# Kernel optimization log

Measured on AMD Instinct MI355X. Metric: run time of the kernel, lower is better.

## Reference

```python
import jax, jax.numpy as jnp
import numpy as np

ALPHA = 0.5        # damping from conf['alpha']
MAX_ITERS = 30     # fixed-point iterations (conf uses up to 150 with eps early-exit)
GN_GROUPS = 3
GN_EPS = 1e-5
SLOPE = 0.01       # F.leaky_relu default negative_slope


def _conv(x, w, b, pad):
    y = jax.lax.conv_general_dilated(
        x, w, window_strides=(1, 1), padding=[(pad, pad), (pad, pad)],
        dimension_numbers=("NCHW", "OIHW", "NCHW"))
    return y + b[None, :, None, None]


def _leaky(x):
    return jnp.where(x >= 0, x, SLOPE * x)


def _groupnorm(x, gamma, beta):
    N, C, H, W = x.shape
    xg = x.reshape(N, GN_GROUPS, C // GN_GROUPS, H, W)
    mu = xg.mean(axis=(2, 3, 4), keepdims=True)
    var = xg.var(axis=(2, 3, 4), keepdims=True)
    xg = (xg - mu) * jax.lax.rsqrt(var + GN_EPS)
    x = xg.reshape(N, C, H, W)
    return x * gamma[None, :, None, None] + beta[None, :, None, None]


def setup_inputs() -> dict:
    key = jax.random.key(0)
    ks = jax.random.split(key, 8)
    image = jax.random.normal(ks[0], (1024, 3, 32, 32), dtype=jnp.float32)
    # Unit params (small init keeps the fixed-point iteration contractive)
    w1 = jax.random.normal(ks[1], (6, 8, 5, 5), dtype=jnp.float32) * 0.05
    b1 = jnp.zeros((6,), jnp.float32)
    gamma = jnp.ones((6,), jnp.float32)
    beta = jnp.zeros((6,), jnp.float32)
    w2 = jax.random.normal(ks[2], (5, 6, 5, 5), dtype=jnp.float32) * 0.05
    b2 = jnp.zeros((5,), jnp.float32)
    # detection head: Conv2d(5, 10, 32, padding=0) -> full-image conv
    wh = jax.random.normal(ks[3], (10, 5, 32, 32), dtype=jnp.float32) * 0.01
    bh = jnp.zeros((10,), jnp.float32)
    return {"image": image, "w1": w1, "b1": b1, "gamma": gamma, "beta": beta,
            "w2": w2, "b2": b2, "wh": wh, "bh": bh}


def reference(image, w1, b1, gamma, beta, w2, b2, wh, bh):
    N = image.shape[0]
    z0 = jnp.zeros((N, 5, 32, 32), image.dtype)

    def unit(z):
        zx = jnp.concatenate([z, image], axis=1)
        h = _groupnorm(_leaky(_conv(zx, w1, b1, 2)), gamma, beta)
        return _leaky(_conv(h, w2, b2, 2))

    def step(z, _):
        z = (1.0 - ALPHA) * z + ALPHA * unit(z)
        return z, None

    z, _ = jax.lax.scan(step, z0, None, length=MAX_ITERS)
    return _conv(z, wh, bh, 0)
```

## Files before the change

kernel.cpp:

```cpp
#include <hip/hip_runtime.h>
#include <hip/hip_fp16.h>


typedef _Float16 half8 __attribute__((ext_vector_type(8)));
typedef float f32x4 __attribute__((ext_vector_type(4)));

__device__ __forceinline__ unsigned pk2(float a, float b) {
    __half2 h = __float22half2_rn(make_float2(a, b));
    return *reinterpret_cast<unsigned*>(&h);
}
__device__ __forceinline__ float2 up2(unsigned u) {
    __half2 h = *reinterpret_cast<__half2*>(&u);
    return __half22float2(h);
}
__device__ __forceinline__ unsigned hmul2(unsigned a, unsigned b) {
    __half2 r = __hmul2(*reinterpret_cast<__half2*>(&a), *reinterpret_cast<__half2*>(&b));
    return *reinterpret_cast<unsigned*>(&r);
}
__device__ __forceinline__ float lrelu(float x) { return fmaxf(x, 0.01f * x); }
__device__ __forceinline__ int bofs(int y, int x) {
    return ((y * 36 + x) * 16) ^ ((x & 8) << 1);
}

__global__ void pack_weights(const float* __restrict__ w1,
                             const float* __restrict__ w2,
                             unsigned* __restrict__ ws)
{
    int t = blockIdx.x * 256 + threadIdx.x;
    if (t < 512) {
        int c = t >> 6, l = t & 63;
        int row = l & 15, tgw = l >> 4;
        int dx = row >> 3, oc = row & 7, tap = 4 * c + tgw;
        unsigned q[4];
        #pragma unroll
        for (int d = 0; d < 4; ++d) {
            float v0 = 0.f, v1 = 0.f;
            if (oc < 6 && tap < 30) {
                int ty = tap / 6, kx = tap % 6 - dx;
                if (kx >= 0 && kx < 5) {
                    v0 = w1[(oc * 8 + 2 * d) * 25 + ty * 5 + kx];
                    v1 = w1[(oc * 8 + 2 * d + 1) * 25 + ty * 5 + kx];
                }
            }
            q[d] = pk2(v0, v1);
        }
        *(uint4*)&ws[t * 4] = make_uint4(q[0], q[1], q[2], q[3]);
    } else if (t < 1024) {
        int u = t - 512;
        int c = u >> 6, l = u & 63;
        int row = l & 15, tgw = l >> 4;
        int dx = row >> 3, oc = row & 7, tap = 4 * c + tgw;
        unsigned q[4];
        #pragma unroll
        for (int d = 0; d < 4; ++d) {
            float v0 = 0.f, v1 = 0.f;
            if (oc < 5 && tap < 30) {
                int ty = tap / 6, kx = tap % 6 - dx;
                if (kx >= 0 && kx < 5) {
                    if (2 * d < 6)     v0 = w2[(oc * 6 + 2 * d) * 25 + ty * 5 + kx];
                    if (2 * d + 1 < 6) v1 = w2[(oc * 6 + 2 * d + 1) * 25 + ty * 5 + kx];
                }
            }
            q[d] = pk2(v0, v1);
        }
        *(uint4*)&ws[2048 + u * 4] = make_uint4(q[0], q[1], q[2], q[3]);
    } else if (t < 1054) {
        int idx = t - 1024;
        int oc = idx / 6, ch = idx % 6;
        float s = 0.f;
        for (int tap = 0; tap < 25; ++tap) s += w2[(oc * 6 + ch) * 25 + tap];
        ((float*)ws)[4096 + idx] = s;
    }
}

__global__ __launch_bounds__(256, 2)
void deq_kernel(const float* __restrict__ image,
                const unsigned* __restrict__ wks,
                const float* __restrict__ b1,
                const float* __restrict__ gam, const float* __restrict__ bet,
                const float* __restrict__ b2,
                const float* __restrict__ wh, const float* __restrict__ bh,
                float* __restrict__ out)
{
    __shared__ __align__(16) unsigned zxb[36 * 36 * 4];
    __shared__ __align__(16) unsigned hbb[36 * 36 * 4];
    __shared__ float red[48];
    __shared__ float s2s[32];

    const int n    = blockIdx.x;
    const int tid  = threadIdx.x;
    const int lane = tid & 63;
    const int wid  = tid >> 6;
    const int col  = lane & 15;
    const int tg   = lane >> 4;
    const int dxl  = tg >> 1;
    const int sub  = tg & 1;

    for (int p = tid; p < 36 * 36 * 4; p += 256) { zxb[p] = 0u; hbb[p] = 0u; }
    if (tid < 30) s2s[tid] = ((const float*)wks)[4096 + tid];
    __syncthreads();

    {
        const int yy = tid >> 3, xx0 = (tid & 7) << 2;
        float4 i0 = *(const float4*)&image[(n * 3 + 0) * 1024 + yy * 32 + xx0];
        float4 i1 = *(const float4*)&image[(n * 3 + 1) * 1024 + yy * 32 + xx0];
        float4 i2 = *(const float4*)&image[(n * 3 + 2) * 1024 + yy * 32 + xx0];
        float a0[4] = {i0.x, i0.y, i0.z, i0.w};
        float a1[4] = {i1.x, i1.y, i1.z, i1.w};
        float a2[4] = {i2.x, i2.y, i2.z, i2.w};
        #pragma unroll
        for (int i = 0; i < 4; ++i) {
            unsigned* bp = (unsigned*)((char*)zxb + bofs(yy + 2, xx0 + 2 + i));
            bp[2] = pk2(0.f, a0[i]);
            bp[3] = pk2(a1[i], a2[i]);
        }
    }

    uint4 cw1[8], cw2[8];
    #pragma unroll
    for (int c = 0; c < 8; ++c) {
        cw1[c] = *(const uint4*)&wks[(c * 64 + lane) * 4];
        cw2[c] = *(const uint4*)&wks[2048 + (c * 64 + lane) * 4];
    }
    int toff[8];
    #pragma unroll
    for (int c = 0; c < 8; ++c) {
        int t = 4 * c + tg;
        int ty = 0, tx = 0;
        if (t < 30) { ty = t / 6; tx = t % 6; }
        int xr = 2 * col + tx;
        toff[c] = ty * 576 + ((xr * 16) ^ ((xr & 8) << 1));
    }

    float b1q[4], b2q[4];
    #pragma unroll
    for (int r = 0; r < 4; ++r) {
        int oc = (tg * 4 + r) & 7;
        b1q[r] = (oc < 6) ? b1[oc] : 0.f;
        b2q[r] = (oc < 5) ? b2[oc] : 0.f;
    }
    const f32x4 ai1 = {b1q[0], b1q[1], b1q[2], b1q[3]};

    __syncthreads();

    const char* zb = (const char*)zxb;
    const char* hb = (const char*)hbb;
    const int ay0 = wid << 3;

    #pragma unroll 1
    for (int it = 0; it < 30; ++it) {
        float ps_lo = 0.f, ps_hi = 0.f, pq_lo = 0.f, pq_hi = 0.f;
        #pragma unroll
        for (int half = 0; half < 2; ++half) {
            const int ayh = ay0 + half * 4;
            f32x4 acc[4];
            #pragma unroll
            for (int g = 0; g < 4; ++g) acc[g] = ai1;
            #pragma unroll
            for (int c = 0; c < 8; ++c) {
                half8 wf = __builtin_bit_cast(half8, cw1[c]);
                #pragma unroll
                for (int g = 0; g < 4; ++g) {
                    half8 pv = *(const half8*)(zb + (ayh + g) * 576 + toff[c]);
                    acc[g] = __builtin_amdgcn_mfma_f32_16x16x32_f16(wf, pv, acc[g], 0, 0, 0);
                }
            }
            #pragma unroll
            for (int g = 0; g < 4; ++g) {
                float h0 = lrelu(acc[g][0]), h1 = lrelu(acc[g][1]);
                float h2 = lrelu(acc[g][2]), h3 = lrelu(acc[g][3]);
                ps_lo += h0 + h1;  pq_lo = fmaf(h0, h0, fmaf(h1, h1, pq_lo));
                ps_hi += h2 + h3;  pq_hi = fmaf(h2, h2, fmaf(h3, h3, pq_hi));
                char* wp = (char*)hbb + bofs(ayh + g + 2, 2 * col + dxl + 2) + sub * 8;
                *(uint2*)wp = make_uint2(pk2(h0, h1), pk2(h2, h3));
            }
        }

        #pragma unroll
        for (int m = 1; m <= 8; m <<= 1) {
            ps_lo += __shfl_xor(ps_lo, m); ps_hi += __shfl_xor(ps_hi, m);
            pq_lo += __shfl_xor(pq_lo, m); pq_hi += __shfl_xor(pq_hi, m);
        }
        ps_lo += __shfl_xor(ps_lo, 32); ps_hi += __shfl_xor(ps_hi, 32);
        pq_lo += __shfl_xor(pq_lo, 32); pq_hi += __shfl_xor(pq_hi, 32);
        if (lane == 0)  { red[wid * 8 + 0] = ps_lo; red[wid * 8 + 1] = ps_hi;
                          red[wid * 8 + 4] = pq_lo; red[wid * 8 + 5] = pq_hi; }
        if (lane == 16) { red[wid * 8 + 2] = ps_lo; red[wid * 8 + 6] = pq_lo; }
        __syncthreads();

        float scv[6], shv[6];
        #pragma unroll
        for (int g3 = 0; g3 < 3; ++g3) {
            float s = 0.f, q = 0.f;
            #pragma unroll
            for (int w = 0; w < 4; ++w) { s += red[w * 8 + g3]; q += red[w * 8 + 4 + g3]; }
            float mean = s * (1.f / 2048.f);
            float var  = q * (1.f / 2048.f) - mean * mean;
            float inv  = rsqrtf(var + 1e-5f);
            #pragma unroll
            for (int k = 0; k < 2; ++k) {
                int c = 2 * g3 + k;
                scv[c] = inv * gam[c];
                shv[c] = bet[c] - mean * scv[c];
            }
        }
        f32x4 ai2;
        #pragma unroll
        for (int r = 0; r < 4; ++r) {
            int ocr = (tg * 4 + r) & 7;
            int base = (ocr < 5) ? ocr * 6 : 0;
            float db = 0.f;
            #pragma unroll
            for (int ch = 0; ch < 6; ++ch) db = fmaf(s2s[base + ch], shv[ch], db);
            ai2[r] = b2q[r] + ((ocr < 5) ? db : 0.f);
        }
        unsigned sp0 = pk2(scv[0], scv[1]), sp1 = pk2(scv[2], scv[3]), sp2 = pk2(scv[4], scv[5]);
        {
            float ph[6];
            #pragma unroll
            for (int c = 0; c < 6; ++c) {
                float rs = (fabsf(scv[c]) > 1e-20f) ? 1.f / scv[c] : 0.f;
                ph[c] = -shv[c] * rs;
            }
            uint4 padq = make_uint4(pk2(ph[0], ph[1]), pk2(ph[2], ph[3]), pk2(ph[4], ph[5]), 0u);
            for (int t = tid; t < 272; t += 256) {
                int row, cc;
                if (t < 72)       { row = t / 36;             cc = t % 36; }
                else if (t < 144) { row = 34 + (t - 72) / 36; cc = (t - 72) % 36; }
                else {
                    int q4 = t - 144;
                    row = 2 + (q4 >> 2);
                    int c4 = q4 & 3;
                    cc = (c4 < 2) ? c4 : c4 + 32;
                }
                *(uint4*)((char*)hbb + bofs(row, cc)) = padq;
            }
        }
        __syncthreads();

        #pragma unroll
        for (int half = 0; half < 2; ++half) {
            const int ayh = ay0 + half * 4;
            f32x4 acc[4];
            #pragma unroll
            for (int g = 0; g < 4; ++g) acc[g] = ai2;
            #pragma unroll
            for (int c = 0; c < 8; ++c) {
                uint4 wsc;
                wsc.x = hmul2(cw2[c].x, sp0);
                wsc.y = hmul2(cw2[c].y, sp1);
                wsc.z = hmul2(cw2[c].z, sp2);
                wsc.w = 0u;
                half8 wf = __builtin_bit_cast(half8, wsc);
                #pragma unroll
                for (int g = 0; g < 4; ++g) {
                    half8 pv = *(const half8*)(hb + (ayh + g) * 576 + toff[c]);
                    acc[g] = __builtin_amdgcn_mfma_f32_16x16x32_f16(wf, pv, acc[g], 0, 0, 0);
                }
            }
            #pragma unroll
            for (int g = 0; g < 4; ++g) {
                char* zp = (char*)zxb + bofs(ayh + g + 2, 2 * col + dxl + 2);
                if (sub == 0) {
                    uint2 zo = *(uint2*)zp;
                    float2 za = up2(zo.x), zc = up2(zo.y);
                    float z0 = 0.5f * za.x + 0.5f * lrelu(acc[g][0]);
                    float z1 = 0.5f * za.y + 0.5f * lrelu(acc[g][1]);
                    float z2 = 0.5f * zc.x + 0.5f * lrelu(acc[g][2]);
                    float z3 = 0.5f * zc.y + 0.5f * lrelu(acc[g][3]);
                    *(uint2*)zp = make_uint2(pk2(z0, z1), pk2(z2, z3));
                } else {
                    _Float16* pz = (_Float16*)(zp + 8);
                    float z4 = 0.5f * (float)pz[0] + 0.5f * lrelu(acc[g][0]);
                    pz[0] = (_Float16)z4;
                }
            }
        }
        __syncthreads();
    }

    {
        const int yy = tid >> 3, xx0 = (tid & 7) << 2;
        float zf[5][4];
        #pragma unroll
        for (int i = 0; i < 4; ++i) {
            const unsigned* bp = (const unsigned*)((const char*)zxb + bofs(yy + 2, xx0 + 2 + i));
            float2 f0 = up2(bp[0]), f1 = up2(bp[1]), f2 = up2(bp[2]);
            zf[0][i] = f0.x; zf[1][i] = f0.y; zf[2][i] = f1.x; zf[3][i] = f1.y; zf[4][i] = f2.x;
        }
        float ho[10];
        #pragma unroll
        for (int o = 0; o < 10; ++o) ho[o] = 0.f;
        #pragma unroll
        for (int c = 0; c < 5; ++c) {
            #pragma unroll
            for (int o = 0; o < 10; ++o) {
                float4 wv = *(const float4*)&wh[(o * 5 + c) * 1024 + yy * 32 + xx0];
                ho[o] = fmaf(zf[c][0], wv.x, ho[o]);
                ho[o] = fmaf(zf[c][1], wv.y, ho[o]);
                ho[o] = fmaf(zf[c][2], wv.z, ho[o]);
                ho[o] = fmaf(zf[c][3], wv.w, ho[o]);
            }
        }
        #pragma unroll
        for (int m = 1; m < 64; m <<= 1) {
            #pragma unroll
            for (int o = 0; o < 10; ++o) ho[o] += __shfl_xor(ho[o], m);
        }
        if (lane == 0) {
            #pragma unroll
            for (int o = 0; o < 10; ++o) red[wid * 10 + o] = ho[o];
        }
    }
    __syncthreads();
    if (tid < 10)
        out[n * 10 + tid] = red[tid] + red[10 + tid] + red[20 + tid] + red[30 + tid] + bh[tid];
}

extern "C" void kernel_launch(void* const* d_in, const int* in_sizes, int n_in,
                              void* d_out, int out_size, void* d_ws, size_t ws_size,
                              hipStream_t stream) {
    const float* image = (const float*)d_in[0];
    const float* w1    = (const float*)d_in[1];
    const float* b1    = (const float*)d_in[2];
    const float* gam   = (const float*)d_in[3];
    const float* bet   = (const float*)d_in[4];
    const float* w2    = (const float*)d_in[5];
    const float* b2    = (const float*)d_in[6];
    const float* wh    = (const float*)d_in[7];
    const float* bh    = (const float*)d_in[8];
    float* out = (float*)d_out;
    unsigned* ws = (unsigned*)d_ws;

    pack_weights<<<5, 256, 0, stream>>>(w1, w2, ws);

    const int N = in_sizes[0] / (3 * 32 * 32);
    deq_kernel<<<N, 256, 0, stream>>>(image, ws, b1, gam, bet, b2, wh, bh, out);
}
```

Before: 356.3 us.

## Switch conv MFMAs to 32x32x16 tiles and apply GroupNorm explicitly

Both 5x5 convolutions now run on 32x32x16 f16 MFMAs instead of 16x16x32 ones. Taps are packed as 8-wide rows over 20 K-chunks, and each wave computes two 4-row tiles with 16-element accumulators. GroupNorm is applied directly to the h values before they are stored to shared memory, replacing the trick of folding the scale into w2 and writing shift-compensated padding values. This removes per-iteration weight scaling and halo rewrites, but zero-padded taps raise the MFMA K work and holding 40 uint4 weight registers adds register pressure.

```diff
diff --git a/kernel.cpp b/kernel.cpp
--- a/kernel.cpp
+++ b/kernel.cpp
@@ -3,7 +3,7 @@
 
 
 typedef _Float16 half8 __attribute__((ext_vector_type(8)));
-typedef float f32x4 __attribute__((ext_vector_type(4)));
+typedef float f32x16 __attribute__((ext_vector_type(16)));
 
 __device__ __forceinline__ unsigned pk2(float a, float b) {
     __half2 h = __float22half2_rn(make_float2(a, b));
@@ -12,10 +12,6 @@
 __device__ __forceinline__ float2 up2(unsigned u) {
     __half2 h = *reinterpret_cast<__half2*>(&u);
     return __half22float2(h);
-}
-__device__ __forceinline__ unsigned hmul2(unsigned a, unsigned b) {
-    __half2 r = __hmul2(*reinterpret_cast<__half2*>(&a), *reinterpret_cast<__half2*>(&b));
-    return *reinterpret_cast<unsigned*>(&r);
 }
 __device__ __forceinline__ float lrelu(float x) { return fmaxf(x, 0.01f * x); }
 __device__ __forceinline__ int bofs(int y, int x) {
@@ -27,49 +23,39 @@
                              unsigned* __restrict__ ws)
 {
     int t = blockIdx.x * 256 + threadIdx.x;
-    if (t < 512) {
+    if (t < 1280) {
         int c = t >> 6, l = t & 63;
-        int row = l & 15, tgw = l >> 4;
-        int dx = row >> 3, oc = row & 7, tap = 4 * c + tgw;
+        int m = l & 31, tp = l >> 5;
+        int dx = m >> 3, oc = m & 7;
+        int tap = 2 * c + tp, ty = tap >> 3, tx = tap & 7, kx = tx - dx;
         unsigned q[4];
         #pragma unroll
         for (int d = 0; d < 4; ++d) {
             float v0 = 0.f, v1 = 0.f;
-            if (oc < 6 && tap < 30) {
-                int ty = tap / 6, kx = tap % 6 - dx;
-                if (kx >= 0 && kx < 5) {
-                    v0 = w1[(oc * 8 + 2 * d) * 25 + ty * 5 + kx];
-                    v1 = w1[(oc * 8 + 2 * d + 1) * 25 + ty * 5 + kx];
-                }
+            if (oc < 6 && kx >= 0 && kx < 5) {
+                v0 = w1[((oc * 8 + 2 * d) * 5 + ty) * 5 + kx];
+                v1 = w1[((oc * 8 + 2 * d + 1) * 5 + ty) * 5 + kx];
             }
             q[d] = pk2(v0, v1);
         }
         *(uint4*)&ws[t * 4] = make_uint4(q[0], q[1], q[2], q[3]);
-    } else if (t < 1024) {
-        int u = t - 512;
+    } else if (t < 2560) {
+        int u = t - 1280;
         int c = u >> 6, l = u & 63;
-        int row = l & 15, tgw = l >> 4;
-        int dx = row >> 3, oc = row & 7, tap = 4 * c + tgw;
+        int m = l & 31, tp = l >> 5;
+        int dx = m >> 3, oc = m & 7;
+        int tap = 2 * c + tp, ty = tap >> 3, tx = tap & 7, kx = tx - dx;
         unsigned q[4];
         #pragma unroll
         for (int d = 0; d < 4; ++d) {
             float v0 = 0.f, v1 = 0.f;
-            if (oc < 5 && tap < 30) {
-                int ty = tap / 6, kx = tap % 6 - dx;
-                if (kx >= 0 && kx < 5) {
-                    if (2 * d < 6)     v0 = w2[(oc * 6 + 2 * d) * 25 + ty * 5 + kx];
-                    if (2 * d + 1 < 6) v1 = w2[(oc * 6 + 2 * d + 1) * 25 + ty * 5 + kx];
-                }
+            if (oc < 5 && kx >= 0 && kx < 5) {
+                if (2 * d < 6)     v0 = w2[((oc * 6 + 2 * d) * 5 + ty) * 5 + kx];
+                if (2 * d + 1 < 6) v1 = w2[((oc * 6 + 2 * d + 1) * 5 + ty) * 5 + kx];
             }
             q[d] = pk2(v0, v1);
         }
-        *(uint4*)&ws[2048 + u * 4] = make_uint4(q[0], q[1], q[2], q[3]);
-    } else if (t < 1054) {
-        int idx = t - 1024;
-        int oc = idx / 6, ch = idx % 6;
-        float s = 0.f;
-        for (int tap = 0; tap < 25; ++tap) s += w2[(oc * 6 + ch) * 25 + tap];
-        ((float*)ws)[4096 + idx] = s;
+        *(uint4*)&ws[5120 + u * 4] = make_uint4(q[0], q[1], q[2], q[3]);
     }
 }
 
@@ -85,19 +71,17 @@
     __shared__ __align__(16) unsigned zxb[36 * 36 * 4];
     __shared__ __align__(16) unsigned hbb[36 * 36 * 4];
     __shared__ float red[48];
-    __shared__ float s2s[32];
 
     const int n    = blockIdx.x;
     const int tid  = threadIdx.x;
     const int lane = tid & 63;
     const int wid  = tid >> 6;
-    const int col  = lane & 15;
-    const int tg   = lane >> 4;
-    const int dxl  = tg >> 1;
-    const int sub  = tg & 1;
+    const int nidx = lane & 31;
+    const int ax   = nidx & 7;
+    const int ry   = nidx >> 3;
+    const int hi   = lane >> 5;
 
     for (int p = tid; p < 36 * 36 * 4; p += 256) { zxb[p] = 0u; hbb[p] = 0u; }
-    if (tid < 30) s2s[tid] = ((const float*)wks)[4096 + tid];
     __syncthreads();
 
     {
@@ -116,79 +100,72 @@
         }
     }
 
-    uint4 cw1[8], cw2[8];
+    uint4 cw1[20], cw2[20];
     #pragma unroll
-    for (int c = 0; c < 8; ++c) {
+    for (int c = 0; c < 20; ++c) {
         cw1[c] = *(const uint4*)&wks[(c * 64 + lane) * 4];
-        cw2[c] = *(const uint4*)&wks[2048 + (c * 64 + lane) * 4];
-    }
-    int toff[8];
+        cw2[c] = *(const uint4*)&wks[5120 + (c * 64 + lane) * 4];
+    }
+    int sx[4];
     #pragma unroll
-    for (int c = 0; c < 8; ++c) {
-        int t = 4 * c + tg;
-        int ty = 0, tx = 0;
-        if (t < 30) { ty = t / 6; tx = t % 6; }
-        int xr = 2 * col + tx;
-        toff[c] = ty * 576 + ((xr * 16) ^ ((xr & 8) << 1));
+    for (int i = 0; i < 4; ++i) {
+        int xr = 4 * ax + hi + 2 * i;
+        sx[i] = (xr * 16) ^ ((xr & 8) << 1);
     }
 
     float b1q[4], b2q[4];
     #pragma unroll
-    for (int r = 0; r < 4; ++r) {
-        int oc = (tg * 4 + r) & 7;
-        b1q[r] = (oc < 6) ? b1[oc] : 0.f;
-        b2q[r] = (oc < 5) ? b2[oc] : 0.f;
-    }
-    const f32x4 ai1 = {b1q[0], b1q[1], b1q[2], b1q[3]};
+    for (int j = 0; j < 4; ++j) {
+        int oc = 4 * hi + j;
+        b1q[j] = (oc < 6) ? b1[oc] : 0.f;
+        b2q[j] = (oc < 5) ? b2[oc] : 0.f;
+    }
 
     __syncthreads();
 
     const char* zb = (const char*)zxb;
     const char* hb = (const char*)hbb;
-    const int ay0 = wid << 3;
+    const int base0 = (wid * 8 + ry) * 576;
+    const int base1 = base0 + 4 * 576;
 
     #pragma unroll 1
     for (int it = 0; it < 30; ++it) {
-        float ps_lo = 0.f, ps_hi = 0.f, pq_lo = 0.f, pq_hi = 0.f;
-        #pragma unroll
-        for (int half = 0; half < 2; ++half) {
-            const int ayh = ay0 + half * 4;
-            f32x4 acc[4];
-            #pragma unroll
-            for (int g = 0; g < 4; ++g) acc[g] = ai1;
-            #pragma unroll
-            for (int c = 0; c < 8; ++c) {
-                half8 wf = __builtin_bit_cast(half8, cw1[c]);
-                #pragma unroll
-                for (int g = 0; g < 4; ++g) {
-                    half8 pv = *(const half8*)(zb + (ayh + g) * 576 + toff[c]);
-                    acc[g] = __builtin_amdgcn_mfma_f32_16x16x32_f16(wf, pv, acc[g], 0, 0, 0);
-                }
-            }
-            #pragma unroll
-            for (int g = 0; g < 4; ++g) {
-                float h0 = lrelu(acc[g][0]), h1 = lrelu(acc[g][1]);
-                float h2 = lrelu(acc[g][2]), h3 = lrelu(acc[g][3]);
-                ps_lo += h0 + h1;  pq_lo = fmaf(h0, h0, fmaf(h1, h1, pq_lo));
-                ps_hi += h2 + h3;  pq_hi = fmaf(h2, h2, fmaf(h3, h3, pq_hi));
-                char* wp = (char*)hbb + bofs(ayh + g + 2, 2 * col + dxl + 2) + sub * 8;
-                *(uint2*)wp = make_uint2(pk2(h0, h1), pk2(h2, h3));
-            }
-        }
-
-        #pragma unroll
-        for (int m = 1; m <= 8; m <<= 1) {
-            ps_lo += __shfl_xor(ps_lo, m); ps_hi += __shfl_xor(ps_hi, m);
-            pq_lo += __shfl_xor(pq_lo, m); pq_hi += __shfl_xor(pq_hi, m);
-        }
-        ps_lo += __shfl_xor(ps_lo, 32); ps_hi += __shfl_xor(ps_hi, 32);
-        pq_lo += __shfl_xor(pq_lo, 32); pq_hi += __shfl_xor(pq_hi, 32);
-        if (lane == 0)  { red[wid * 8 + 0] = ps_lo; red[wid * 8 + 1] = ps_hi;
-                          red[wid * 8 + 4] = pq_lo; red[wid * 8 + 5] = pq_hi; }
-        if (lane == 16) { red[wid * 8 + 2] = ps_lo; red[wid * 8 + 6] = pq_lo; }
+        f32x16 acc[2];
+        #pragma unroll
+        for (int g = 0; g < 2; ++g)
+            #pragma unroll
+            for (int r = 0; r < 16; ++r) acc[g][r] = b1q[r & 3];
+        #pragma unroll
+        for (int c = 0; c < 20; ++c) {
+            half8 wf = __builtin_bit_cast(half8, cw1[c]);
+            const int off = (c >> 2) * 576 + sx[c & 3];
+            half8 p0 = *(const half8*)(zb + base0 + off);
+            acc[0] = __builtin_amdgcn_mfma_f32_32x32x16_f16(wf, p0, acc[0], 0, 0, 0);
+            half8 p1 = *(const half8*)(zb + base1 + off);
+            acc[1] = __builtin_amdgcn_mfma_f32_32x32x16_f16(wf, p1, acc[1], 0, 0, 0);
+        }
+
+        float ps_a = 0.f, pq_a = 0.f, ps_b = 0.f, pq_b = 0.f;
+        #pragma unroll
+        for (int g = 0; g < 2; ++g)
+            #pragma unroll
+            for (int r = 0; r < 16; ++r) {
+                float v = lrelu(acc[g][r]);
+                acc[g][r] = v;
+                if ((r & 3) < 2) { ps_a += v; pq_a = fmaf(v, v, pq_a); }
+                else             { ps_b += v; pq_b = fmaf(v, v, pq_b); }
+            }
+        #pragma unroll
+        for (int m = 1; m <= 16; m <<= 1) {
+            ps_a += __shfl_xor(ps_a, m); pq_a += __shfl_xor(pq_a, m);
+            ps_b += __shfl_xor(ps_b, m); pq_b += __shfl_xor(pq_b, m);
+        }
+        if (lane == 0)  { red[wid * 8 + 0] = ps_a; red[wid * 8 + 1] = ps_b;
+                          red[wid * 8 + 4] = pq_a; red[wid * 8 + 5] = pq_b; }
+        if (lane == 32) { red[wid * 8 + 2] = ps_a; red[wid * 8 + 6] = pq_a; }
         __syncthreads();
 
-        float scv[6], shv[6];
+        float scv[8], shv[8];
         #pragma unroll
         for (int g3 = 0; g3 < 3; ++g3) {
             float s = 0.f, q = 0.f;
@@ -204,74 +181,54 @@
                 shv[c] = bet[c] - mean * scv[c];
             }
         }
-        f32x4 ai2;
-        #pragma unroll
-        for (int r = 0; r < 4; ++r) {
-            int ocr = (tg * 4 + r) & 7;
-            int base = (ocr < 5) ? ocr * 6 : 0;
-            float db = 0.f;
-            #pragma unroll
-            for (int ch = 0; ch < 6; ++ch) db = fmaf(s2s[base + ch], shv[ch], db);
-            ai2[r] = b2q[r] + ((ocr < 5) ? db : 0.f);
-        }
-        unsigned sp0 = pk2(scv[0], scv[1]), sp1 = pk2(scv[2], scv[3]), sp2 = pk2(scv[4], scv[5]);
-        {
-            float ph[6];
-            #pragma unroll
-            for (int c = 0; c < 6; ++c) {
-                float rs = (fabsf(scv[c]) > 1e-20f) ? 1.f / scv[c] : 0.f;
-                ph[c] = -shv[c] * rs;
-            }
-            uint4 padq = make_uint4(pk2(ph[0], ph[1]), pk2(ph[2], ph[3]), pk2(ph[4], ph[5]), 0u);
-            for (int t = tid; t < 272; t += 256) {
-                int row, cc;
-                if (t < 72)       { row = t / 36;             cc = t % 36; }
-                else if (t < 144) { row = 34 + (t - 72) / 36; cc = (t - 72) % 36; }
-                else {
-                    int q4 = t - 144;
-                    row = 2 + (q4 >> 2);
-                    int c4 = q4 & 3;
-                    cc = (c4 < 2) ? c4 : c4 + 32;
-                }
-                *(uint4*)((char*)hbb + bofs(row, cc)) = padq;
+        scv[6] = scv[7] = shv[6] = shv[7] = 0.f;
+
+        #pragma unroll
+        for (int g = 0; g < 2; ++g) {
+            const int yrow = wid * 8 + g * 4 + ry + 2;
+            #pragma unroll
+            for (int d = 0; d < 4; ++d) {
+                float h0 = fmaf(acc[g][4 * d + 0], scv[4 * hi + 0], shv[4 * hi + 0]);
+                float h1 = fmaf(acc[g][4 * d + 1], scv[4 * hi + 1], shv[4 * hi + 1]);
+                float h2 = fmaf(acc[g][4 * d + 2], scv[4 * hi + 2], shv[4 * hi + 2]);
+                float h3 = fmaf(acc[g][4 * d + 3], scv[4 * hi + 3], shv[4 * hi + 3]);
+                char* wp = (char*)hbb + bofs(yrow, 4 * ax + d + 2) + hi * 8;
+                *(uint2*)wp = make_uint2(pk2(h0, h1), pk2(h2, h3));
             }
         }
         __syncthreads();
 
         #pragma unroll
-        for (int half = 0; half < 2; ++half) {
-            const int ayh = ay0 + half * 4;
-            f32x4 acc[4];
-            #pragma unroll
-            for (int g = 0; g < 4; ++g) acc[g] = ai2;
-            #pragma unroll
-            for (int c = 0; c < 8; ++c) {
-                uint4 wsc;
-                wsc.x = hmul2(cw2[c].x, sp0);
-                wsc.y = hmul2(cw2[c].y, sp1);
-                wsc.z = hmul2(cw2[c].z, sp2);
-                wsc.w = 0u;
-                half8 wf = __builtin_bit_cast(half8, wsc);
-                #pragma unroll
-                for (int g = 0; g < 4; ++g) {
-                    half8 pv = *(const half8*)(hb + (ayh + g) * 576 + toff[c]);
-                    acc[g] = __builtin_amdgcn_mfma_f32_16x16x32_f16(wf, pv, acc[g], 0, 0, 0);
-                }
-            }
-            #pragma unroll
-            for (int g = 0; g < 4; ++g) {
-                char* zp = (char*)zxb + bofs(ayh + g + 2, 2 * col + dxl + 2);
-                if (sub == 0) {
+        for (int g = 0; g < 2; ++g)
+            #pragma unroll
+            for (int r = 0; r < 16; ++r) acc[g][r] = b2q[r & 3];
+        #pragma unroll
+        for (int c = 0; c < 20; ++c) {
+            half8 wf = __builtin_bit_cast(half8, cw2[c]);
+            const int off = (c >> 2) * 576 + sx[c & 3];
+            half8 p0 = *(const half8*)(hb + base0 + off);
+            acc[0] = __builtin_amdgcn_mfma_f32_32x32x16_f16(wf, p0, acc[0], 0, 0, 0);
+            half8 p1 = *(const half8*)(hb + base1 + off);
+            acc[1] = __builtin_amdgcn_mfma_f32_32x32x16_f16(wf, p1, acc[1], 0, 0, 0);
+        }
+
+        #pragma unroll
+        for (int g = 0; g < 2; ++g) {
+            const int yrow = wid * 8 + g * 4 + ry + 2;
+            #pragma unroll
+            for (int d = 0; d < 4; ++d) {
+                char* zp = (char*)zxb + bofs(yrow, 4 * ax + d + 2);
+                if (hi == 0) {
                     uint2 zo = *(uint2*)zp;
                     float2 za = up2(zo.x), zc = up2(zo.y);
-                    float z0 = 0.5f * za.x + 0.5f * lrelu(acc[g][0]);
-                    float z1 = 0.5f * za.y + 0.5f * lrelu(acc[g][1]);
-                    float z2 = 0.5f * zc.x + 0.5f * lrelu(acc[g][2]);
-                    float z3 = 0.5f * zc.y + 0.5f * lrelu(acc[g][3]);
+                    float z0 = 0.5f * za.x + 0.5f * lrelu(acc[g][4 * d + 0]);
+                    float z1 = 0.5f * za.y + 0.5f * lrelu(acc[g][4 * d + 1]);
+                    float z2 = 0.5f * zc.x + 0.5f * lrelu(acc[g][4 * d + 2]);
+                    float z3 = 0.5f * zc.y + 0.5f * lrelu(acc[g][4 * d + 3]);
                     *(uint2*)zp = make_uint2(pk2(z0, z1), pk2(z2, z3));
                 } else {
                     _Float16* pz = (_Float16*)(zp + 8);
-                    float z4 = 0.5f * (float)pz[0] + 0.5f * lrelu(acc[g][0]);
+                    float z4 = 0.5f * (float)pz[0] + 0.5f * lrelu(acc[g][4 * d + 0]);
                     pz[0] = (_Float16)z4;
                 }
             }
@@ -332,7 +289,7 @@
     float* out = (float*)d_out;
     unsigned* ws = (unsigned*)d_ws;
 
-    pack_weights<<<5, 256, 0, stream>>>(w1, w2, ws);
+    pack_weights<<<10, 256, 0, stream>>>(w1, w2, ws);
 
     const int N = in_sizes[0] / (3 * 32 * 32);
     deq_kernel<<<N, 256, 0, stream>>>(image, ws, b1, gam, bet, b2, wh, bh, out);
```

After: 438.5 us. 23.1% more time.
